# Kernel optimization log

Hardware: AMD Instinct MI355X
Metric: run time of the kernel (lower is better)

The kernel has to match this reference:

```python
import math
import jax, jax.numpy as jnp
import numpy as np

NUM_COEFFS = 64
REPEAT = 4
IN_CH = 256
OUT_CH = 256
BATCH = 8
SEQ_L = 8192


def setup_inputs() -> dict:
    key = jax.random.key(0)
    k1, k2 = jax.random.split(key)
    n = NUM_COEFFS * REPEAT
    # S4D-style init, exactly as in the torch __init__
    log_A_real = np.log(np.exp(0.5) - 1.0) * np.ones(NUM_COEFFS)
    A_imag = math.pi * np.arange(NUM_COEFFS)
    A = np.tile(np.stack([log_A_real, A_imag], -1), (REPEAT, 1))  # [n, 2]
    B = np.ones((n, IN_CH)) / math.sqrt(IN_CH)                    # [n, c_in]
    log_dt = np.repeat(np.linspace(np.log(0.001), np.log(0.1), REPEAT), NUM_COEFFS)  # [n]
    C = jax.random.normal(k1, (OUT_CH, n), dtype=jnp.float32) * math.sqrt(2.0 / n)
    x = jax.random.normal(k2, (BATCH, IN_CH, SEQ_L), dtype=jnp.float32)
    return {
        "x": x,
        "A": jnp.asarray(A, dtype=jnp.float32),
        "B": jnp.asarray(B, dtype=jnp.float32),
        "log_dt": jnp.asarray(log_dt, dtype=jnp.float32),
        "C": C,
    }


def _fft_conv_bnl(x, K):
    # Causal/linear convolution via zero-padded FFT of length 2L, keep first L.
    # x: [b, n, l], K: [n, l] -> [b, n, l]
    l = x.shape[-1]
    xf = jnp.fft.rfft(x, 2 * l)
    kf = jnp.fft.rfft(K, 2 * l)
    y = jnp.fft.irfft(xf * kf, 2 * l)
    return y[..., :l]


def reference(x, A, B, log_dt, C):
    L = x.shape[-1]
    # ssm_basis_kernels
    log_A_real, A_imag = A[:, 0], A[:, 1]          # [n]
    lrange = jnp.arange(L, dtype=x.dtype)          # [L]
    dt = jnp.exp(log_dt)                           # [n]
    dtA_real = -dt * jax.nn.softplus(log_A_real)
    dtA_imag = dt * A_imag
    K = jnp.exp(dtA_real[:, None] * lrange) * jnp.cos(dtA_imag[:, None] * lrange)  # [n, L]
    B_hat = B * dt[:, None]                        # [n, c_in]
    # opt_ssm_forward: with these shapes the torch code takes the coeffs<=c_in branch
    xb = jnp.einsum('bcl,nc->bnl', x, B_hat)       # project into state basis
    y = _fft_conv_bnl(xb, K)                       # per-state long conv via FFT
    return jnp.einsum('bnl,dn->bdl', y, C)         # project to output channels
```

## Files before the change

kernel.cpp:

```cpp
#include <hip/hip_runtime.h>
#include <hip/hip_bf16.h>
#include <math.h>

#define BATCH 8
#define L_SEQ 8192
#define KD    256

typedef __attribute__((ext_vector_type(8))) short bf16x8;
typedef __attribute__((ext_vector_type(4))) float f32x4;

__device__ __forceinline__ void async_ld16(const __hip_bfloat16* g, __hip_bfloat16* l) {
    __builtin_amdgcn_global_load_lds(
        (const __attribute__((address_space(1))) unsigned int*)g,
        (__attribute__((address_space(3))) unsigned int*)l, 16, 0, 0);
}

__global__ void prep(const float* __restrict__ B, const float* __restrict__ logdt,
                     const float* __restrict__ C,
                     __hip_bfloat16* __restrict__ W1bf, __hip_bfloat16* __restrict__ Cbf) {
    int i = blockIdx.x * 256 + threadIdx.x;
    W1bf[i] = __float2bfloat16(B[i] * expf(logdt[i >> 8]));
    Cbf[i]  = __float2bfloat16(C[i]);
}

__global__ __launch_bounds__(256) void transpose_cast(
        const float* __restrict__ X, __hip_bfloat16* __restrict__ XT) {
    __shared__ float tile[64][65];
    const int t = threadIdx.x;
    const int l0 = blockIdx.x * 64, c0 = blockIdx.y * 64, b = blockIdx.z;
    const float* Xb = X + (size_t)b * KD * L_SEQ;
    __hip_bfloat16* Tb = XT + (size_t)b * L_SEQ * KD;

    int cl = t >> 4;
    int l4 = (t & 15) * 4;
#pragma unroll
    for (int i = 0; i < 4; ++i) {
        int c = cl + 16 * i;
        float4 v = *(const float4*)(Xb + (size_t)(c0 + c) * L_SEQ + l0 + l4);
        tile[c][l4 + 0] = v.x; tile[c][l4 + 1] = v.y;
        tile[c][l4 + 2] = v.z; tile[c][l4 + 3] = v.w;
    }
    __syncthreads();

    int ll = t & 63;
    int c8g = t >> 6;
#pragma unroll
    for (int h = 0; h < 2; ++h) {
        int c8 = (c8g + 4 * h) * 8;
        union { __hip_bfloat16 s[8]; uint4 v; } pk;
#pragma unroll
        for (int j = 0; j < 8; ++j) pk.s[j] = __float2bfloat16(tile[c8 + j][ll]);
        *(uint4*)(Tb + (size_t)(l0 + ll) * KD + c0 + c8) = pk.v;
    }
}

template <typename OutT>
__global__ __launch_bounds__(256) void mfma_gemm(
        const __hip_bfloat16* __restrict__ Ag,
        const __hip_bfloat16* __restrict__ Bg,
        OutT* __restrict__ Dg,
        int nrows, int ncols, long Abstride, long Bbstride)
{
    __shared__ __hip_bfloat16 Abuf[16 * 512];
    __shared__ __hip_bfloat16 Bbuf[16 * 512];

    const int t = threadIdx.x, lane = t & 63, wave = t >> 6;
    const int wr = wave >> 1, wc = wave & 1;
    const int row0 = blockIdx.y * 128, col0 = blockIdx.x * 128;
    const int lm = lane & 15, lq = lane >> 4;
    const __hip_bfloat16* Ab = Ag + (size_t)blockIdx.z * Abstride;
    const __hip_bfloat16* Bb = Bg + (size_t)blockIdx.z * Bbstride;
    OutT* Db = Dg + (size_t)blockIdx.z * (size_t)nrows * ncols;

    f32x4 acc[4][4];
#pragma unroll
    for (int i = 0; i < 4; ++i)
#pragma unroll
        for (int j = 0; j < 4; ++j) acc[i][j] = {0.f, 0.f, 0.f, 0.f};

    for (int k0 = 0; k0 < KD; k0 += 64) {
#pragma unroll
        for (int i = 0; i < 8; ++i) {
            int idx = wave * 8 + i;
            if (idx < 16) {
                int rt = idx >> 1, s = idx & 1;
                const __hip_bfloat16* g =
                    Ab + (size_t)(row0 + rt * 16 + lm) * KD + k0 + s * 32 + lq * 8;
                async_ld16(g, &Abuf[idx * 512 + lane * 8]);
            } else {
                int jb = idx - 16, ct = jb >> 1, s = jb & 1;
                const __hip_bfloat16* g =
                    Bb + (size_t)(col0 + ct * 16 + lm) * KD + k0 + s * 32 + lq * 8;
                async_ld16(g, &Bbuf[jb * 512 + lane * 8]);
            }
        }
        __syncthreads();
#pragma unroll
        for (int s = 0; s < 2; ++s) {
            bf16x8 af[4], bfr[4];
#pragma unroll
            for (int i = 0; i < 4; ++i)
                af[i] = *(const bf16x8*)&Abuf[((wr * 4 + i) * 2 + s) * 512 + lane * 8];
#pragma unroll
            for (int j = 0; j < 4; ++j)
                bfr[j] = *(const bf16x8*)&Bbuf[((wc * 4 + j) * 2 + s) * 512 + lane * 8];
#pragma unroll
            for (int i = 0; i < 4; ++i)
#pragma unroll
                for (int j = 0; j < 4; ++j)
                    acc[i][j] = __builtin_amdgcn_mfma_f32_16x16x32_bf16(
                        af[i], bfr[j], acc[i][j], 0, 0, 0);
        }
        __syncthreads();
    }

#pragma unroll
    for (int i = 0; i < 4; ++i) {
        int r0 = row0 + wr * 64 + i * 16 + lq * 4;
#pragma unroll
        for (int j = 0; j < 4; ++j) {
            int c = col0 + wc * 64 + j * 16 + lm;
#pragma unroll
            for (int r = 0; r < 4; ++r)
                Db[(size_t)(r0 + r) * ncols + c] = (OutT)acc[i][j][r];
        }
    }
}

__device__ __forceinline__ void lambda_of(const float* A, const float* logdt, int n,
                                          float& lr, float& li, float& dAr, float& dAi) {
    float dt = expf(logdt[n]);
    dAr = -dt * log1pf(expf(A[2 * n]));
    dAi = dt * A[2 * n + 1];
    float e = expf(dAr);
    lr = e * cosf(dAi);
    li = e * sinf(dAi);
}

__global__ __launch_bounds__(256) void scan_sum(
        const __hip_bfloat16* __restrict__ xb, const float* __restrict__ A,
        const float* __restrict__ logdt, float2* __restrict__ sums) {
    const int n = threadIdx.x, seg = blockIdx.x, b = blockIdx.y;
    float lr, li, dAr, dAi;
    lambda_of(A, logdt, n, lr, li, dAr, dAi);
    const __hip_bfloat16* p = xb + ((size_t)b * L_SEQ + seg * 128) * KD + n;
    float sr = 0.f, si = 0.f;
#pragma unroll 4
    for (int l = 0; l < 128; ++l) {
        float v = __bfloat162float(p[(size_t)l * KD]);
        float nr = lr * sr - li * si + v;
        float ni = lr * si + li * sr;
        sr = nr; si = ni;
    }
    sums[((size_t)b * KD + n) * 64 + seg] = make_float2(sr, si);
}

__global__ __launch_bounds__(64) void scan_carry(
        const float* __restrict__ A, const float* __restrict__ logdt,
        float2* __restrict__ sums) {
    const int lane = threadIdx.x;
    const int b = blockIdx.x >> 8, n = blockIdx.x & 255;
    float lr, li, dAr, dAi;
    lambda_of(A, logdt, n, lr, li, dAr, dAi);
    float er = expf(dAr * 128.0f), ph = dAi * 128.0f;
    float mr = er * cosf(ph), mi = er * sinf(ph);

    float2 s = sums[((size_t)b * KD + n) * 64 + lane];
    float vr = s.x, vi = s.y;
#pragma unroll
    for (int d = 1; d < 64; d <<= 1) {
        float ur = __shfl_up(vr, (unsigned)d);
        float ui = __shfl_up(vi, (unsigned)d);
        if (lane >= d) {
            float tr = mr * ur - mi * ui + vr;
            float ti = mr * ui + mi * ur + vi;
            vr = tr; vi = ti;
        }
        float m2r = mr * mr - mi * mi;
        float m2i = 2.0f * mr * mi;
        mr = m2r; mi = m2i;
    }
    float cr = __shfl_up(vr, 1u), ci = __shfl_up(vi, 1u);
    if (lane == 0) { cr = 0.f; ci = 0.f; }
    sums[((size_t)b * KD + n) * 64 + lane] = make_float2(cr, ci);
}

__global__ __launch_bounds__(256) void scan_apply(
        __hip_bfloat16* __restrict__ xb, const float* __restrict__ A,
        const float* __restrict__ logdt, const float2* __restrict__ sums) {
    const int n = threadIdx.x, seg = blockIdx.x, b = blockIdx.y;
    float lr, li, dAr, dAi;
    lambda_of(A, logdt, n, lr, li, dAr, dAi);
    float2 c = sums[((size_t)b * KD + n) * 64 + seg];
    float sr = c.x, si = c.y;
    __hip_bfloat16* p = xb + ((size_t)b * L_SEQ + seg * 128) * KD + n;
#pragma unroll 4
    for (int l = 0; l < 128; ++l) {
        float v = __bfloat162float(p[(size_t)l * KD]);
        float nr = lr * sr - li * si + v;
        float ni = lr * si + li * sr;
        sr = nr; si = ni;
        p[(size_t)l * KD] = __float2bfloat16(nr);
    }
}

extern "C" void kernel_launch(void* const* d_in, const int* in_sizes, int n_in,
                              void* d_out, int out_size, void* d_ws, size_t ws_size,
                              hipStream_t stream) {
    const float* x      = (const float*)d_in[0];
    const float* A      = (const float*)d_in[1];
    const float* B      = (const float*)d_in[2];
    const float* log_dt = (const float*)d_in[3];
    const float* C      = (const float*)d_in[4];
    float* out = (float*)d_out;

    char* ws = (char*)d_ws;
    __hip_bfloat16* W1bf = (__hip_bfloat16*)(ws);
    __hip_bfloat16* Cbf  = (__hip_bfloat16*)(ws + (128 << 10));
    float2*         sums = (float2*)(ws + (256 << 10));
    __hip_bfloat16* x_t  = (__hip_bfloat16*)(ws + (1280 << 10));
    __hip_bfloat16* xb_t = (__hip_bfloat16*)(ws + (1280 << 10) + ((size_t)32 << 20));

    const long PB = (long)L_SEQ * KD;

    prep<<<256, 256, 0, stream>>>(B, log_dt, C, W1bf, Cbf);
    transpose_cast<<<dim3(L_SEQ / 64, KD / 64, BATCH), 256, 0, stream>>>(x, x_t);
    mfma_gemm<__hip_bfloat16><<<dim3(KD / 128, L_SEQ / 128, BATCH), 256, 0, stream>>>(
        x_t, W1bf, xb_t, L_SEQ, KD, PB, 0);
    scan_sum<<<dim3(64, BATCH), 256, 0, stream>>>(xb_t, A, log_dt, sums);
    scan_carry<<<BATCH * KD, 64, 0, stream>>>(A, log_dt, sums);
    scan_apply<<<dim3(64, BATCH), 256, 0, stream>>>(xb_t, A, log_dt, sums);
    mfma_gemm<float><<<dim3(L_SEQ / 128, KD / 128, BATCH), 256, 0, stream>>>(
        Cbf, xb_t, out, KD, L_SEQ, 0, PB);
}
```

Measured before the change: 203.7 us.

## Fuse transpose-cast and segment scan sums into first GEMM, parallelize scan apply

Removes the separate transpose_cast kernel by loading fp32 x directly in the first GEMM, converting to bf16 and writing a swizzled LDS tile. The per-segment scan partial sums are computed in the GEMM epilogue from fp32 accumulators using precomputed decay weights, which removes the scan_sum pass over xb. scan_apply now uses vectorized 8-channel loads with a two-level in-block scan over 16-step sub-segments, and a lambda table is precomputed once in prep. This cuts global memory traffic and kernel count, at the cost of more epilogue math (exp/cos/sin) and slightly different rounding, since partial sums now use fp32 values instead of bf16.

```diff
diff --git a/kernel.cpp b/kernel.cpp
--- a/kernel.cpp
+++ b/kernel.cpp
@@ -16,50 +16,261 @@
 }
 
 __global__ void prep(const float* __restrict__ B, const float* __restrict__ logdt,
-                     const float* __restrict__ C,
-                     __hip_bfloat16* __restrict__ W1bf, __hip_bfloat16* __restrict__ Cbf) {
+                     const float* __restrict__ C, const float* __restrict__ A,
+                     __hip_bfloat16* __restrict__ W1bf, __hip_bfloat16* __restrict__ Cbf,
+                     float2* __restrict__ lamtab) {
     int i = blockIdx.x * 256 + threadIdx.x;
     W1bf[i] = __float2bfloat16(B[i] * expf(logdt[i >> 8]));
     Cbf[i]  = __float2bfloat16(C[i]);
-}
-
-__global__ __launch_bounds__(256) void transpose_cast(
-        const float* __restrict__ X, __hip_bfloat16* __restrict__ XT) {
-    __shared__ float tile[64][65];
+    if (blockIdx.x == 0) {
+        int n = threadIdx.x;
+        float dt  = expf(logdt[n]);
+        float dAr = -dt * log1pf(expf(A[2 * n]));
+        float dAi = dt * A[2 * n + 1];
+        float e1 = expf(dAr);
+        lamtab[n * 4 + 0] = make_float2(e1 * cosf(dAi), e1 * sinf(dAi));
+        float e16 = expf(16.f * dAr);
+        lamtab[n * 4 + 1] = make_float2(e16 * cosf(16.f * dAi), e16 * sinf(16.f * dAi));
+        float e128 = expf(128.f * dAr);
+        lamtab[n * 4 + 2] = make_float2(e128 * cosf(128.f * dAi), e128 * sinf(128.f * dAi));
+        lamtab[n * 4 + 3] = make_float2(dAr, dAi);
+    }
+}
+
+__global__ __launch_bounds__(256) void gemm1(
+        const float* __restrict__ X, const __hip_bfloat16* __restrict__ W1,
+        const float2* __restrict__ lamtab,
+        __hip_bfloat16* __restrict__ XBT, float2* __restrict__ sums)
+{
+    __shared__ __hip_bfloat16 Abuf[16 * 512];
+    __shared__ __hip_bfloat16 Bbuf[16 * 512];
+
+    const int t = threadIdx.x, lane = t & 63, wave = t >> 6;
+    const int wr = wave >> 1, wc = wave & 1;
+    const int lm = lane & 15, lq = lane >> 4;
+    const int seg = blockIdx.y;
+    const int row0 = seg * 128;
+    const int col0 = blockIdx.x * 128;
+    const int b = blockIdx.z;
+    const float* Xb = X + (size_t)b * KD * L_SEQ;
+
+    const int c8  = t >> 5;
+    const int l4  = (t & 31) * 4;
+    const int s_w = c8 >> 2;
+    const int lq_w = c8 & 3;
+
+    f32x4 acc[4][4];
+#pragma unroll
+    for (int i = 0; i < 4; ++i)
+#pragma unroll
+        for (int j = 0; j < 4; ++j) acc[i][j] = {0.f, 0.f, 0.f, 0.f};
+
+    for (int k0 = 0; k0 < KD; k0 += 64) {
+#pragma unroll
+        for (int i = 0; i < 4; ++i) {
+            int jb = wave * 4 + i, ct = jb >> 1, sB = jb & 1;
+            const __hip_bfloat16* g =
+                W1 + (size_t)(col0 + ct * 16 + lm) * KD + k0 + sB * 32 + lq * 8;
+            async_ld16(g, &Bbuf[jb * 512 + lane * 8]);
+        }
+        float4 xv[8];
+#pragma unroll
+        for (int i = 0; i < 8; ++i)
+            xv[i] = *(const float4*)(Xb + (size_t)(k0 + c8 * 8 + i) * L_SEQ + row0 + l4);
+#pragma unroll
+        for (int j = 0; j < 4; ++j) {
+            int l = l4 + j;
+            int rt = l >> 4, lmW = l & 15;
+            union { __hip_bfloat16 h[8]; uint4 u; } pk;
+#pragma unroll
+            for (int i = 0; i < 8; ++i) {
+                const float* f = (const float*)&xv[i];
+                pk.h[i] = __float2bfloat16(f[j]);
+            }
+            int slot = (lmW ^ rt ^ (s_w << 3)) + 16 * lq_w;
+            *(uint4*)&Abuf[(rt * 2 + s_w) * 512 + slot * 8] = pk.u;
+        }
+        __syncthreads();
+#pragma unroll
+        for (int s = 0; s < 2; ++s) {
+            bf16x8 af[4], bfr[4];
+#pragma unroll
+            for (int i = 0; i < 4; ++i) {
+                int rt = wr * 4 + i;
+                int slot = (lm ^ rt ^ (s << 3)) + 16 * lq;
+                af[i] = *(const bf16x8*)&Abuf[(rt * 2 + s) * 512 + slot * 8];
+            }
+#pragma unroll
+            for (int j = 0; j < 4; ++j)
+                bfr[j] = *(const bf16x8*)&Bbuf[((wc * 4 + j) * 2 + s) * 512 + lane * 8];
+#pragma unroll
+            for (int i = 0; i < 4; ++i)
+#pragma unroll
+                for (int j = 0; j < 4; ++j)
+                    acc[i][j] = __builtin_amdgcn_mfma_f32_16x16x32_bf16(
+                        af[i], bfr[j], acc[i][j], 0, 0, 0);
+        }
+        __syncthreads();
+    }
+
+    __hip_bfloat16* Db = XBT + (size_t)b * L_SEQ * KD;
+#pragma unroll
+    for (int i = 0; i < 4; ++i) {
+        int r0 = row0 + wr * 64 + i * 16 + lq * 4;
+#pragma unroll
+        for (int j = 0; j < 4; ++j) {
+            int c = col0 + wc * 64 + j * 16 + lm;
+#pragma unroll
+            for (int r = 0; r < 4; ++r)
+                Db[(size_t)(r0 + r) * KD + c] = __float2bfloat16(acc[i][j][r]);
+        }
+    }
+
+    float2 par[4];
+#pragma unroll
+    for (int j = 0; j < 4; ++j) {
+        int n = col0 + wc * 64 + j * 16 + lm;
+        float2 dA  = lamtab[n * 4 + 3];
+        float2 lam = lamtab[n * 4 + 0];
+        float m1r = lam.x, m1i = lam.y;
+        float sr = 0.f, si = 0.f;
+#pragma unroll
+        for (int i = 0; i < 4; ++i) {
+            int lbase = wr * 64 + i * 16 + lq * 4;
+            float p = (float)(127 - lbase - 3);
+            float er = expf(dA.x * p);
+            float wrr = er * cosf(dA.y * p), wii = er * sinf(dA.y * p);
+            for (int r = 3; r >= 0; --r) {
+                float v = acc[i][j][r];
+                sr += wrr * v; si += wii * v;
+                float nr = wrr * m1r - wii * m1i;
+                float ni = wrr * m1i + wii * m1r;
+                wrr = nr; wii = ni;
+            }
+        }
+        sr += __shfl_xor(sr, 16); si += __shfl_xor(si, 16);
+        sr += __shfl_xor(sr, 32); si += __shfl_xor(si, 32);
+        par[j] = make_float2(sr, si);
+    }
+    float2* ssum = (float2*)Bbuf;
+    if (wr == 0 && lq == 0) {
+#pragma unroll
+        for (int j = 0; j < 4; ++j) ssum[wc * 64 + j * 16 + lm] = par[j];
+    }
+    __syncthreads();
+    if (wr == 1 && lq == 0) {
+#pragma unroll
+        for (int j = 0; j < 4; ++j) {
+            float2 o = ssum[wc * 64 + j * 16 + lm];
+            int n = col0 + wc * 64 + j * 16 + lm;
+            sums[((size_t)b * KD + n) * 64 + seg] =
+                make_float2(par[j].x + o.x, par[j].y + o.y);
+        }
+    }
+}
+
+__global__ __launch_bounds__(64) void scan_carry(
+        const float2* __restrict__ lamtab, float2* __restrict__ sums) {
+    const int lane = threadIdx.x;
+    const int b = blockIdx.x >> 8, n = blockIdx.x & 255;
+    float2 m = lamtab[n * 4 + 2];
+    float mr = m.x, mi = m.y;
+    float2 s = sums[((size_t)b * KD + n) * 64 + lane];
+    float vr = s.x, vi = s.y;
+#pragma unroll
+    for (int d = 1; d < 64; d <<= 1) {
+        float ur = __shfl_up(vr, (unsigned)d);
+        float ui = __shfl_up(vi, (unsigned)d);
+        if (lane >= d) {
+            float tr = mr * ur - mi * ui + vr;
+            float ti = mr * ui + mi * ur + vi;
+            vr = tr; vi = ti;
+        }
+        float m2r = mr * mr - mi * mi;
+        float m2i = 2.0f * mr * mi;
+        mr = m2r; mi = m2i;
+    }
+    float cr = __shfl_up(vr, 1u), ci = __shfl_up(vi, 1u);
+    if (lane == 0) { cr = 0.f; ci = 0.f; }
+    sums[((size_t)b * KD + n) * 64 + lane] = make_float2(cr, ci);
+}
+
+__global__ __launch_bounds__(256) void scan_apply(
+        __hip_bfloat16* __restrict__ XBT, const float2* __restrict__ lamtab,
+        const float2* __restrict__ sums)
+{
+    __shared__ float2 sl[8][258];
     const int t = threadIdx.x;
-    const int l0 = blockIdx.x * 64, c0 = blockIdx.y * 64, b = blockIdx.z;
-    const float* Xb = X + (size_t)b * KD * L_SEQ;
-    __hip_bfloat16* Tb = XT + (size_t)b * L_SEQ * KD;
-
-    int cl = t >> 4;
-    int l4 = (t & 15) * 4;
-#pragma unroll
-    for (int i = 0; i < 4; ++i) {
-        int c = cl + 16 * i;
-        float4 v = *(const float4*)(Xb + (size_t)(c0 + c) * L_SEQ + l0 + l4);
-        tile[c][l4 + 0] = v.x; tile[c][l4 + 1] = v.y;
-        tile[c][l4 + 2] = v.z; tile[c][l4 + 3] = v.w;
-    }
+    const int sub = t >> 5, n0 = (t & 31) * 8;
+    const int seg = blockIdx.x, b = blockIdx.y;
+    __hip_bfloat16* base = XBT + ((size_t)b * L_SEQ + seg * 128 + sub * 16) * KD + n0;
+
+    float2 lam[8];
+#pragma unroll
+    for (int k = 0; k < 8; ++k) lam[k] = lamtab[(n0 + k) * 4];
+
+    uint4 xv[16];
+    float sr[8], si[8];
+#pragma unroll
+    for (int k = 0; k < 8; ++k) { sr[k] = 0.f; si[k] = 0.f; }
+
+#pragma unroll
+    for (int l = 0; l < 16; ++l) {
+        xv[l] = *(const uint4*)(base + (size_t)l * KD);
+        const __hip_bfloat16* xs = (const __hip_bfloat16*)&xv[l];
+#pragma unroll
+        for (int k = 0; k < 8; ++k) {
+            float v = __bfloat162float(xs[k]);
+            float nr = lam[k].x * sr[k] - lam[k].y * si[k] + v;
+            float ni = lam[k].x * si[k] + lam[k].y * sr[k];
+            sr[k] = nr; si[k] = ni;
+        }
+    }
+#pragma unroll
+    for (int k = 0; k < 8; ++k) sl[sub][n0 + k] = make_float2(sr[k], si[k]);
     __syncthreads();
 
-    int ll = t & 63;
-    int c8g = t >> 6;
-#pragma unroll
-    for (int h = 0; h < 2; ++h) {
-        int c8 = (c8g + 4 * h) * 8;
-        union { __hip_bfloat16 s[8]; uint4 v; } pk;
-#pragma unroll
-        for (int j = 0; j < 8; ++j) pk.s[j] = __float2bfloat16(tile[c8 + j][ll]);
-        *(uint4*)(Tb + (size_t)(l0 + ll) * KD + c0 + c8) = pk.v;
-    }
-}
-
-template <typename OutT>
-__global__ __launch_bounds__(256) void mfma_gemm(
+    {
+        int n = t;
+        float2 m16 = lamtab[n * 4 + 1];
+        float2 c = sums[((size_t)b * KD + n) * 64 + seg];
+        float cr = c.x, ci = c.y;
+#pragma unroll
+        for (int s2 = 0; s2 < 8; ++s2) {
+            float2 loc = sl[s2][n];
+            sl[s2][n] = make_float2(cr, ci);
+            float nr = m16.x * cr - m16.y * ci + loc.x;
+            float ni = m16.x * ci + m16.y * cr + loc.y;
+            cr = nr; ci = ni;
+        }
+    }
+    __syncthreads();
+
+#pragma unroll
+    for (int k = 0; k < 8; ++k) {
+        float2 c = sl[sub][n0 + k];
+        sr[k] = c.x; si[k] = c.y;
+    }
+#pragma unroll
+    for (int l = 0; l < 16; ++l) {
+        const __hip_bfloat16* xs = (const __hip_bfloat16*)&xv[l];
+        union { __hip_bfloat16 h[8]; uint4 u; } yv;
+#pragma unroll
+        for (int k = 0; k < 8; ++k) {
+            float v = __bfloat162float(xs[k]);
+            float nr = lam[k].x * sr[k] - lam[k].y * si[k] + v;
+            float ni = lam[k].x * si[k] + lam[k].y * sr[k];
+            sr[k] = nr; si[k] = ni;
+            yv.h[k] = __float2bfloat16(nr);
+        }
+        *(uint4*)(base + (size_t)l * KD) = yv.u;
+    }
+}
+
+__global__ __launch_bounds__(256) void gemm2(
         const __hip_bfloat16* __restrict__ Ag,
         const __hip_bfloat16* __restrict__ Bg,
-        OutT* __restrict__ Dg,
-        int nrows, int ncols, long Abstride, long Bbstride)
+        float* __restrict__ Dg)
 {
     __shared__ __hip_bfloat16 Abuf[16 * 512];
     __shared__ __hip_bfloat16 Bbuf[16 * 512];
@@ -68,9 +279,8 @@
     const int wr = wave >> 1, wc = wave & 1;
     const int row0 = blockIdx.y * 128, col0 = blockIdx.x * 128;
     const int lm = lane & 15, lq = lane >> 4;
-    const __hip_bfloat16* Ab = Ag + (size_t)blockIdx.z * Abstride;
-    const __hip_bfloat16* Bb = Bg + (size_t)blockIdx.z * Bbstride;
-    OutT* Db = Dg + (size_t)blockIdx.z * (size_t)nrows * ncols;
+    const __hip_bfloat16* Bb = Bg + (size_t)blockIdx.z * L_SEQ * KD;
+    float* Db = Dg + (size_t)blockIdx.z * KD * L_SEQ;
 
     f32x4 acc[4][4];
 #pragma unroll
@@ -85,7 +295,7 @@
             if (idx < 16) {
                 int rt = idx >> 1, s = idx & 1;
                 const __hip_bfloat16* g =
-                    Ab + (size_t)(row0 + rt * 16 + lm) * KD + k0 + s * 32 + lq * 8;
+                    Ag + (size_t)(row0 + rt * 16 + lm) * KD + k0 + s * 32 + lq * 8;
                 async_ld16(g, &Abuf[idx * 512 + lane * 8]);
             } else {
                 int jb = idx - 16, ct = jb >> 1, s = jb & 1;
@@ -122,85 +332,8 @@
             int c = col0 + wc * 64 + j * 16 + lm;
 #pragma unroll
             for (int r = 0; r < 4; ++r)
-                Db[(size_t)(r0 + r) * ncols + c] = (OutT)acc[i][j][r];
-        }
-    }
-}
-
-__device__ __forceinline__ void lambda_of(const float* A, const float* logdt, int n,
-                                          float& lr, float& li, float& dAr, float& dAi) {
-    float dt = expf(logdt[n]);
-    dAr = -dt * log1pf(expf(A[2 * n]));
-    dAi = dt * A[2 * n + 1];
-    float e = expf(dAr);
-    lr = e * cosf(dAi);
-    li = e * sinf(dAi);
-}
-
-__global__ __launch_bounds__(256) void scan_sum(
-        const __hip_bfloat16* __restrict__ xb, const float* __restrict__ A,
-        const float* __restrict__ logdt, float2* __restrict__ sums) {
-    const int n = threadIdx.x, seg = blockIdx.x, b = blockIdx.y;
-    float lr, li, dAr, dAi;
-    lambda_of(A, logdt, n, lr, li, dAr, dAi);
-    const __hip_bfloat16* p = xb + ((size_t)b * L_SEQ + seg * 128) * KD + n;
-    float sr = 0.f, si = 0.f;
-#pragma unroll 4
-    for (int l = 0; l < 128; ++l) {
-        float v = __bfloat162float(p[(size_t)l * KD]);
-        float nr = lr * sr - li * si + v;
-        float ni = lr * si + li * sr;
-        sr = nr; si = ni;
-    }
-    sums[((size_t)b * KD + n) * 64 + seg] = make_float2(sr, si);
-}
-
-__global__ __launch_bounds__(64) void scan_carry(
-        const float* __restrict__ A, const float* __restrict__ logdt,
-        float2* __restrict__ sums) {
-    const int lane = threadIdx.x;
-    const int b = blockIdx.x >> 8, n = blockIdx.x & 255;
-    float lr, li, dAr, dAi;
-    lambda_of(A, logdt, n, lr, li, dAr, dAi);
-    float er = expf(dAr * 128.0f), ph = dAi * 128.0f;
-    float mr = er * cosf(ph), mi = er * sinf(ph);
-
-    float2 s = sums[((size_t)b * KD + n) * 64 + lane];
-    float vr = s.x, vi = s.y;
-#pragma unroll
-    for (int d = 1; d < 64; d <<= 1) {
-        float ur = __shfl_up(vr, (unsigned)d);
-        float ui = __shfl_up(vi, (unsigned)d);
-        if (lane >= d) {
-            float tr = mr * ur - mi * ui + vr;
-            float ti = mr * ui + mi * ur + vi;
-            vr = tr; vi = ti;
-        }
-        float m2r = mr * mr - mi * mi;
-        float m2i = 2.0f * mr * mi;
-        mr = m2r; mi = m2i;
-    }
-    float cr = __shfl_up(vr, 1u), ci = __shfl_up(vi, 1u);
-    if (lane == 0) { cr = 0.f; ci = 0.f; }
-    sums[((size_t)b * KD + n) * 64 + lane] = make_float2(cr, ci);
-}
-
-__global__ __launch_bounds__(256) void scan_apply(
-        __hip_bfloat16* __restrict__ xb, const float* __restrict__ A,
-        const float* __restrict__ logdt, const float2* __restrict__ sums) {
-    const int n = threadIdx.x, seg = blockIdx.x, b = blockIdx.y;
-    float lr, li, dAr, dAi;
-    lambda_of(A, logdt, n, lr, li, dAr, dAi);
-    float2 c = sums[((size_t)b * KD + n) * 64 + seg];
-    float sr = c.x, si = c.y;
-    __hip_bfloat16* p = xb + ((size_t)b * L_SEQ + seg * 128) * KD + n;
-#pragma unroll 4
-    for (int l = 0; l < 128; ++l) {
-        float v = __bfloat162float(p[(size_t)l * KD]);
-        float nr = lr * sr - li * si + v;
-        float ni = lr * si + li * sr;
-        sr = nr; si = ni;
-        p[(size_t)l * KD] = __float2bfloat16(nr);
+                Db[(size_t)(r0 + r) * L_SEQ + c] = acc[i][j][r];
+        }
     }
 }
 
@@ -217,19 +350,13 @@
     char* ws = (char*)d_ws;
     __hip_bfloat16* W1bf = (__hip_bfloat16*)(ws);
     __hip_bfloat16* Cbf  = (__hip_bfloat16*)(ws + (128 << 10));
-    float2*         sums = (float2*)(ws + (256 << 10));
-    __hip_bfloat16* x_t  = (__hip_bfloat16*)(ws + (1280 << 10));
-    __hip_bfloat16* xb_t = (__hip_bfloat16*)(ws + (1280 << 10) + ((size_t)32 << 20));
-
-    const long PB = (long)L_SEQ * KD;
-
-    prep<<<256, 256, 0, stream>>>(B, log_dt, C, W1bf, Cbf);
-    transpose_cast<<<dim3(L_SEQ / 64, KD / 64, BATCH), 256, 0, stream>>>(x, x_t);
-    mfma_gemm<__hip_bfloat16><<<dim3(KD / 128, L_SEQ / 128, BATCH), 256, 0, stream>>>(
-        x_t, W1bf, xb_t, L_SEQ, KD, PB, 0);
-    scan_sum<<<dim3(64, BATCH), 256, 0, stream>>>(xb_t, A, log_dt, sums);
-    scan_carry<<<BATCH * KD, 64, 0, stream>>>(A, log_dt, sums);
-    scan_apply<<<dim3(64, BATCH), 256, 0, stream>>>(xb_t, A, log_dt, sums);
-    mfma_gemm<float><<<dim3(L_SEQ / 128, KD / 128, BATCH), 256, 0, stream>>>(
-        Cbf, xb_t, out, KD, L_SEQ, 0, PB);
-}
+    float2*         lamtab = (float2*)(ws + (256 << 10));
+    float2*         sums = (float2*)(ws + (320 << 10));
+    __hip_bfloat16* xb_t = (__hip_bfloat16*)(ws + ((size_t)2 << 20));
+
+    prep<<<256, 256, 0, stream>>>(B, log_dt, C, A, W1bf, Cbf, lamtab);
+    gemm1<<<dim3(2, 64, BATCH), 256, 0, stream>>>(x, W1bf, lamtab, xb_t, sums);
+    scan_carry<<<BATCH * KD, 64, 0, stream>>>(lamtab, sums);
+    scan_apply<<<dim3(64, BATCH), 256, 0, stream>>>(xb_t, lamtab, sums);
+    gemm2<<<dim3(L_SEQ / 128, KD / 128, BATCH), 256, 0, stream>>>(Cbf, xb_t, out);
+}
```

Result: faster. 180.9 us (-11.2%).
